# Performance work log

Measured on AMD Instinct MI355X. Metric: run time of the kernel, lower is better.

## Reference

```python
import jax, jax.numpy as jnp
import numpy as np

N_NODES = 100000


def _sage_conv(x, src, dst, Wl, bl, Wr):
    # PyG SAGEConv (aggr='mean', root_weight=True):
    # out_i = Wl @ mean_{j in N(i)} x_j + bl + Wr @ x_i
    msg = x[src]                                              # [E, F] gather
    s = jax.ops.segment_sum(msg, dst, num_segments=N_NODES)   # [N, F] scatter-add
    cnt = jax.ops.segment_sum(jnp.ones((src.shape[0], 1), x.dtype), dst,
                              num_segments=N_NODES)           # [N, 1]
    mean = s / jnp.maximum(cnt, 1.0)                          # empty nbhd -> 0
    return mean @ Wl + bl + x @ Wr


def setup_inputs() -> dict:
    key = jax.random.key(0)
    ks = jax.random.split(key, 8)
    N, E, F = N_NODES, 1600000, 128
    x = jax.random.normal(ks[0], (N, F), dtype=jnp.float32)
    edge_index = jax.random.randint(ks[1], (2, E), 0, N, dtype=jnp.int64)
    def lin(k, fi, fo):
        return jax.random.normal(k, (fi, fo), dtype=jnp.float32) / np.sqrt(fi)
    return {
        "x": x, "edge_index": edge_index,
        "Wl0": lin(ks[2], F, F), "bl0": jnp.zeros((F,), jnp.float32), "Wr0": lin(ks[3], F, F),
        "Wl1": lin(ks[4], F, F), "bl1": jnp.zeros((F,), jnp.float32), "Wr1": lin(ks[5], F, F),
        "Wl2": lin(ks[6], F, F), "bl2": jnp.zeros((F,), jnp.float32), "Wr2": lin(ks[7], F, F),
    }


def reference(x, edge_index, Wl0, bl0, Wr0, Wl1, bl1, Wr1, Wl2, bl2, Wr2):
    src, dst = edge_index[0], edge_index[1]
    # layers 0..num_layers-2: SAGEConv -> ReLU -> dropout(eval=identity)
    h = jax.nn.relu(_sage_conv(x, src, dst, Wl0, bl0, Wr0))
    h = jax.nn.relu(_sage_conv(h, src, dst, Wl1, bl1, Wr1))
    # final layer: no activation
    out = _sage_conv(h, src, dst, Wl2, bl2, Wr2)
    return out
```

## Files before the change

### kernel.cpp

```cpp
#include <hip/hip_runtime.h>
#include <stdint.h>

#define NN 100000
#define FF 128
#define NB 391

typedef __bf16 bf16x8 __attribute__((ext_vector_type(8)));
typedef float f32x4 __attribute__((ext_vector_type(4)));

__device__ __forceinline__ unsigned short f2bf(float f) {
    unsigned int u = __float_as_uint(f);
    u += 0x7FFF + ((u >> 16) & 1);
    return (unsigned short)(u >> 16);
}
__device__ __forceinline__ float bf2f(unsigned short b) {
    return __uint_as_float(((unsigned int)b) << 16);
}

__device__ __forceinline__ int edge_at(const void* ei, int idx, int is64) {
    if (is64) return (int)((const long long*)ei)[idx];
    return ((const int*)ei)[idx];
}

__global__ void init_kernel(const unsigned int* ei, int* flag, int* bcnt) {
    __shared__ int any;
    int t = threadIdx.x;
    if (t == 0) any = 0;
    for (int i = t; i < NB; i += 512) bcnt[i] = 0;
    __syncthreads();
    unsigned int v = ei[2 * t + 1];
    if (v != 0u) atomicOr(&any, 1);
    __syncthreads();
    if (t == 0) *flag = (any ? 0 : 1);
}

__global__ void bcount_prep_kernel(const void* ei, const int* flag, int* bcnt, int E,
                                   const float* __restrict__ x, unsigned short* __restrict__ xb,
                                   const float* Wl0, const float* Wr0,
                                   const float* Wl1, const float* Wr1,
                                   const float* Wl2, const float* Wr2,
                                   unsigned short* __restrict__ whi) {
    if (blockIdx.x < 256) {
        __shared__ int h[NB];
        for (int i = threadIdx.x; i < NB; i += 256) h[i] = 0;
        __syncthreads();
        int is64 = *flag;
        int stride = 256 * 256;
        for (int e = blockIdx.x * 256 + threadIdx.x; e < E; e += stride)
            atomicAdd(&h[edge_at(ei, E + e, is64) >> 8], 1);
        __syncthreads();
        for (int i = threadIdx.x; i < NB; i += 256) {
            int v = h[i];
            if (v) atomicAdd(&bcnt[i], v);
        }
    } else {
        int gid = (blockIdx.x - 256) * 256 + threadIdx.x;
        int gstride = (gridDim.x - 256) * 256;
        const int PC = NN * FF / 8;
        for (int i = gid; i < PC; i += gstride) {
            float4 a = ((const float4*)x)[i * 2];
            float4 b = ((const float4*)x)[i * 2 + 1];
            ushort4 p0 = make_ushort4(f2bf(a.x), f2bf(a.y), f2bf(a.z), f2bf(a.w));
            ushort4 p1 = make_ushort4(f2bf(b.x), f2bf(b.y), f2bf(b.z), f2bf(b.w));
            ((ushort4*)xb)[i * 2] = p0;
            ((ushort4*)xb)[i * 2 + 1] = p1;
        }
        const int WT = 3 * 256 * FF;
        for (int i = gid; i < WT; i += gstride) {
            int l = i >> 15;
            int rem = i & 32767;
            int n = rem >> 7;
            int k = rem & 127;
            const float* Wl = l == 0 ? Wl0 : (l == 1 ? Wl1 : Wl2);
            const float* Wr = l == 0 ? Wr0 : (l == 1 ? Wr1 : Wr2);
            float v = (n < FF) ? Wl[k * FF + n] : Wr[k * FF + (n - FF)];
            whi[i] = f2bf(v);
        }
    }
}

__global__ void bscan_kernel(const int* bcnt, int* bbase, int* bcursor,
                             int* rowptr, int E) {
    __shared__ int s[512];
    int t = threadIdx.x;
    int v = (t < NB) ? bcnt[t] : 0;
    s[t] = v;
    __syncthreads();
    for (int off = 1; off < 512; off <<= 1) {
        int u = (t >= off) ? s[t - off] : 0;
        __syncthreads();
        s[t] += u;
        __syncthreads();
    }
    if (t <= NB) {
        int excl = (t == 0) ? 0 : s[t - 1];
        bbase[t] = excl;
        if (t < NB) bcursor[t] = excl;
    }
    if (t == 0) rowptr[NN] = E;
}

__global__ void bscatter_kernel(const void* ei, const int* flag, int* bcursor,
                                unsigned int* packed, int E, int CH) {
    __shared__ int cnt[NB];
    __shared__ int base[NB];
    int t = threadIdx.x;
    for (int i = t; i < NB; i += 256) cnt[i] = 0;
    __syncthreads();
    int is64 = *flag;
    int beg = blockIdx.x * CH;
    int end = min(E, beg + CH);
    for (int e = beg + t; e < end; e += 256)
        atomicAdd(&cnt[edge_at(ei, E + e, is64) >> 8], 1);
    __syncthreads();
    for (int i = t; i < NB; i += 256) {
        int c = cnt[i];
        base[i] = c ? atomicAdd(&bcursor[i], c) : 0;
    }
    __syncthreads();
    for (int i = t; i < NB; i += 256) cnt[i] = 0;
    __syncthreads();
    for (int e = beg + t; e < end; e += 256) {
        int sV = edge_at(ei, e, is64);
        int d  = edge_at(ei, E + e, is64);
        int b = d >> 8;
        int pos = base[b] + atomicAdd(&cnt[b], 1);
        packed[pos] = ((unsigned int)sV << 8) | (unsigned int)(d & 255);
    }
}

__global__ void bfill_kernel(const unsigned int* __restrict__ packed,
                             const int* __restrict__ bbase,
                             int* __restrict__ rowptr, int* __restrict__ col) {
    __shared__ int cnt[256];
    __shared__ int scn[256];
    __shared__ int exc[256];
    int t = threadIdx.x;
    int b = blockIdx.x;
    int ebeg = bbase[b], eend = bbase[b + 1];
    cnt[t] = 0;
    __syncthreads();
    for (int e = ebeg + t; e < eend; e += 256)
        atomicAdd(&cnt[packed[e] & 255], 1);
    __syncthreads();
    int v = cnt[t];
    scn[t] = v;
    __syncthreads();
    for (int off = 1; off < 256; off <<= 1) {
        int u = (t >= off) ? scn[t - off] : 0;
        __syncthreads();
        scn[t] += u;
        __syncthreads();
    }
    int excl = scn[t] - v;
    exc[t] = excl;
    int node = b * 256 + t;
    if (node < NN) rowptr[node] = ebeg + excl;
    cnt[t] = 0;
    __syncthreads();
    for (int e = ebeg + t; e < eend; e += 256) {
        unsigned int p = packed[e];
        int l = p & 255;
        int pos = ebeg + exc[l] + atomicAdd(&cnt[l], 1);
        col[pos] = (int)(p >> 8);
    }
}

__device__ __forceinline__ unsigned int rowld(const unsigned short* __restrict__ h,
                                              int c, int lbyte) {
    return *(const unsigned int*)((const char*)h + ((size_t)(unsigned)c << 8) + lbyte);
}

__global__ void aggregate_kernel(const unsigned short* __restrict__ h,
                                 const int* __restrict__ rowptr,
                                 const int* __restrict__ col,
                                 unsigned short* __restrict__ m) {
    int gw = (int)((blockIdx.x * blockDim.x + threadIdx.x) >> 6);
    gw = __builtin_amdgcn_readfirstlane(gw);
    if (gw >= NN) return;
    const int lane = (int)(threadIdx.x & 63);
    const int lbyte = lane * 4;
    int beg = __builtin_amdgcn_readfirstlane(rowptr[gw]);
    int end = __builtin_amdgcn_readfirstlane(rowptr[gw + 1]);
    int deg = end - beg;
    float a0 = 0.f, a1 = 0.f;

    int done = 0;
    while (done < deg) {
        int batch = min(deg - done, 64);
        int colv = 0;
        if (lane < batch) colv = col[beg + done + lane];
        unsigned int u0 = 0, u1 = 0, u2 = 0, u3 = 0;
        u0 = rowld(h, __builtin_amdgcn_readlane(colv, 0), lbyte);
        if (batch > 1) u1 = rowld(h, __builtin_amdgcn_readlane(colv, 1), lbyte);
        if (batch > 2) u2 = rowld(h, __builtin_amdgcn_readlane(colv, 2), lbyte);
        if (batch > 3) u3 = rowld(h, __builtin_amdgcn_readlane(colv, 3), lbyte);
        for (int i = 0; i < batch; i += 4) {
            unsigned int n0 = 0, n1 = 0, n2 = 0, n3 = 0;
            if (i + 4 < batch) n0 = rowld(h, __builtin_amdgcn_readlane(colv, i + 4), lbyte);
            if (i + 5 < batch) n1 = rowld(h, __builtin_amdgcn_readlane(colv, i + 5), lbyte);
            if (i + 6 < batch) n2 = rowld(h, __builtin_amdgcn_readlane(colv, i + 6), lbyte);
            if (i + 7 < batch) n3 = rowld(h, __builtin_amdgcn_readlane(colv, i + 7), lbyte);
            a0 += __uint_as_float(u0 << 16);
            a1 += __uint_as_float(u0 & 0xffff0000u);
            a0 += __uint_as_float(u1 << 16);
            a1 += __uint_as_float(u1 & 0xffff0000u);
            a0 += __uint_as_float(u2 << 16);
            a1 += __uint_as_float(u2 & 0xffff0000u);
            a0 += __uint_as_float(u3 << 16);
            a1 += __uint_as_float(u3 & 0xffff0000u);
            u0 = n0; u1 = n1; u2 = n2; u3 = n3;
        }
        done += batch;
    }

    float r = deg > 0 ? 1.f / (float)deg : 0.f;
    unsigned int p = (unsigned int)f2bf(a0 * r) | ((unsigned int)f2bf(a1 * r) << 16);
    *(unsigned int*)((char*)m + ((size_t)gw << 8) + lbyte) = p;
}

template <int WMODE>
__global__ __launch_bounds__(256, 6) void gemm_mfma_kernel(
        const unsigned short* __restrict__ mb,
        const unsigned short* __restrict__ hb,
        const unsigned short* __restrict__ w2,
        const float* __restrict__ bl,
        void* __restrict__ outp) {
    __shared__ __align__(16) char smem[16384];

    const int t = threadIdx.x;
    const int lane = t & 63;
    const int wid = t >> 6;
    const int m0 = blockIdx.x * 64;
    const int n0w = wid * 32;

    f32x4 acc[4][2];
    #pragma unroll
    for (int mr = 0; mr < 4; ++mr)
        #pragma unroll
        for (int nr = 0; nr < 2; ++nr) acc[mr][nr] = (f32x4){0.f, 0.f, 0.f, 0.f};

    const int srow = t >> 2;
    const int sk8 = (t & 3) * 8;
    const int arow = lane & 15;
    const int kg = (lane >> 4) * 8;

    uint4 pfM, pfH;
    auto issueA = [&](int kc) {
        int gr = m0 + srow; if (gr >= NN) gr = NN - 1;
        size_t ga = (size_t)gr * FF + kc * 32 + sk8;
        pfM = *(const uint4*)(mb + ga);
        pfH = *(const uint4*)(hb + ga);
    };

    issueA(0);
    for (int kc = 0; kc < 4; ++kc) {
        __syncthreads();
        *(uint4*)(smem +        srow * 80 + sk8 * 2) = pfM;
        *(uint4*)(smem + 5120 + srow * 80 + sk8 * 2) = pfH;
        if (kc < 3) issueA(kc + 1);
        __syncthreads();

        bf16x8 wfrag[4];
        #pragma unroll
        for (int nr = 0; nr < 2; ++nr) {
            int n = n0w + nr * 16 + arow;
            wfrag[nr * 2 + 0] = *(const bf16x8*)(w2 + (size_t)n * FF + kc * 32 + kg);
            wfrag[nr * 2 + 1] = *(const bf16x8*)(w2 + (size_t)(128 + n) * FF + kc * 32 + kg);
        }
        const int kg2 = (lane >> 4) * 16;
        #pragma unroll
        for (int mr = 0; mr < 4; ++mr) {
            int row = mr * 16 + arow;
            bf16x8 a_m = *(const bf16x8*)(smem +        row * 80 + kg2);
            bf16x8 a_h = *(const bf16x8*)(smem + 5120 + row * 80 + kg2);
            #pragma unroll
            for (int nr = 0; nr < 2; ++nr) {
                acc[mr][nr] = __builtin_amdgcn_mfma_f32_16x16x32_bf16(wfrag[nr * 2 + 0], a_m, acc[mr][nr], 0, 0, 0);
                acc[mr][nr] = __builtin_amdgcn_mfma_f32_16x16x32_bf16(wfrag[nr * 2 + 1], a_h, acc[mr][nr], 0, 0, 0);
            }
        }
    }

    const int nodeL = lane & 15;
    const int rg4 = (lane >> 4) * 4;
    if (WMODE == 0) {
        __syncthreads();
        #pragma unroll
        for (int nr = 0; nr < 2; ++nr) {
            int n = n0w + nr * 16 + rg4;
            float4 bias = *(const float4*)(bl + n);
            int g = n >> 2;
            #pragma unroll
            for (int mr = 0; mr < 4; ++mr) {
                int row = mr * 16 + nodeL;
                f32x4 a = acc[mr][nr];
                float o0 = fmaxf(a[0] + bias.x, 0.f), o1 = fmaxf(a[1] + bias.y, 0.f);
                float o2 = fmaxf(a[2] + bias.z, 0.f), o3 = fmaxf(a[3] + bias.w, 0.f);
                ushort4 p = make_ushort4(f2bf(o0), f2bf(o1), f2bf(o2), f2bf(o3));
                *(ushort4*)(smem + row * 256 + ((g ^ ((row & 7) << 2)) << 3)) = p;
            }
        }
        __syncthreads();
        unsigned short* hout = (unsigned short*)outp;
        #pragma unroll
        for (int it = 0; it < 8; ++it) {
            int idx = t + it * 256;
            int row = idx >> 5;
            int g = idx & 31;
            int node = m0 + row;
            if (node < NN) {
                ushort4 v = *(const ushort4*)(smem + row * 256 + ((g ^ ((row & 7) << 2)) << 3));
                *(ushort4*)(hout + (size_t)node * FF + g * 4) = v;
            }
        }
    } else {
        float* fout = (float*)outp;
        #pragma unroll
        for (int r = 0; r < 2; ++r) {
            __syncthreads();
            #pragma unroll
            for (int nr = 0; nr < 2; ++nr) {
                int n = n0w + nr * 16 + rg4;
                float4 bias = *(const float4*)(bl + n);
                int g = n >> 2;
                #pragma unroll
                for (int mr = 2 * r; mr < 2 * r + 2; ++mr) {
                    int lrow = mr * 16 + nodeL - 32 * r;
                    f32x4 a = acc[mr][nr];
                    float4 p = make_float4(a[0] + bias.x, a[1] + bias.y,
                                           a[2] + bias.z, a[3] + bias.w);
                    *(float4*)(smem + lrow * 512 + ((g ^ (lrow & 7)) << 4)) = p;
                }
            }
            __syncthreads();
            #pragma unroll
            for (int it = 0; it < 4; ++it) {
                int idx = t + it * 256;
                int lrow = idx >> 5;
                int g = idx & 31;
                int node = m0 + 32 * r + lrow;
                if (node < NN) {
                    float4 v = *(const float4*)(smem + lrow * 512 + ((g ^ (lrow & 7)) << 4));
                    *(float4*)(fout + (size_t)node * FF + g * 4) = v;
                }
            }
        }
    }
}

extern "C" void kernel_launch(void* const* d_in, const int* in_sizes, int n_in,
                              void* d_out, int out_size, void* d_ws, size_t ws_size,
                              hipStream_t stream) {
    const float* x   = (const float*)d_in[0];
    const void*  ei  = d_in[1];
    const float* Wl0 = (const float*)d_in[2];
    const float* bl0 = (const float*)d_in[3];
    const float* Wr0 = (const float*)d_in[4];
    const float* Wl1 = (const float*)d_in[5];
    const float* bl1 = (const float*)d_in[6];
    const float* Wr1 = (const float*)d_in[7];
    const float* Wl2 = (const float*)d_in[8];
    const float* bl2 = (const float*)d_in[9];
    const float* Wr2 = (const float*)d_in[10];
    float* out = (float*)d_out;
    const int E = in_sizes[1] / 2;

    char* w = (char*)d_ws;
    size_t off = 0;
    auto alloc = [&](size_t bytes) {
        void* p = w + off;
        off += (bytes + 511) & ~(size_t)511;
        return p;
    };
    int*            flag    = (int*)alloc(4);
    int*            bcnt    = (int*)alloc(sizeof(int) * NB);
    int*            bbase   = (int*)alloc(sizeof(int) * (NB + 1));
    int*            bcursor = (int*)alloc(sizeof(int) * NB);
    int*            rowptr  = (int*)alloc(sizeof(int) * (NN + 1));
    unsigned int*   packed  = (unsigned int*)alloc(sizeof(int) * E);
    int*            col     = (int*)alloc(sizeof(int) * E);
    unsigned short* whi     = (unsigned short*)alloc(sizeof(short) * 3 * 256 * FF);
    unsigned short* xb      = (unsigned short*)alloc(sizeof(short) * (size_t)NN * FF);
    unsigned short* mbuf    = (unsigned short*)alloc(sizeof(short) * (size_t)NN * FF);
    unsigned short* hA      = (unsigned short*)alloc(sizeof(short) * (size_t)NN * FF);
    unsigned short* hB      = xb;

    init_kernel<<<1, 512, 0, stream>>>((const unsigned int*)ei, flag, bcnt);
    bcount_prep_kernel<<<1280, 256, 0, stream>>>(ei, flag, bcnt, E,
                                                 x, xb, Wl0, Wr0, Wl1, Wr1, Wl2, Wr2, whi);
    bscan_kernel<<<1, 512, 0, stream>>>(bcnt, bbase, bcursor, rowptr, E);
    int CH = (E + 255) / 256;
    bscatter_kernel<<<256, 256, 0, stream>>>(ei, flag, bcursor, packed, E, CH);
    bfill_kernel<<<NB, 256, 0, stream>>>(packed, bbase, rowptr, col);

    int gb = (NN + 63) / 64;
    int ab = (NN * 64 + 255) / 256;

    aggregate_kernel<<<ab, 256, 0, stream>>>(xb, rowptr, col, mbuf);
    gemm_mfma_kernel<0><<<gb, 256, 0, stream>>>(mbuf, xb, whi + 0 * 256 * FF, bl0, hA);
    aggregate_kernel<<<ab, 256, 0, stream>>>(hA, rowptr, col, mbuf);
    gemm_mfma_kernel<0><<<gb, 256, 0, stream>>>(mbuf, hA, whi + 1 * 256 * FF, bl1, hB);
    aggregate_kernel<<<ab, 256, 0, stream>>>(hB, rowptr, col, mbuf);
    gemm_mfma_kernel<1><<<gb, 256, 0, stream>>>(mbuf, hB, whi + 2 * 256 * FF, bl2, out);
}
```

Before: 309.0 us.

## Slice bf16 feature storage into 8 column slabs and aggregate per slab

Feature matrices are now stored as 8 slabs of 16 columns each (32 bytes per node), and the aggregate kernel assigns each block a single slab, so each slab's working set (about 3.2 MB) can stay resident in cache during the random gathers. Each wave now handles 8 destination nodes with 8 lanes each, and prefetches column indices with nontemporal loads up to the group's maximum degree. The GEMM's input loads and bf16 output writes are changed to the slab layout. In exchange, each gather is only 32 bytes wide, column indices are re-read once per slab, and lanes idle while their node waits on the highest-degree node in its group.

```diff
diff --git a/kernel.cpp b/kernel.cpp
--- a/kernel.cpp
+++ b/kernel.cpp
@@ -4,6 +4,8 @@
 #define NN 100000
 #define FF 128
 #define NB 391
+#define NSL 8
+#define SLW 16
 
 typedef __bf16 bf16x8 __attribute__((ext_vector_type(8)));
 typedef float f32x4 __attribute__((ext_vector_type(4)));
@@ -22,11 +24,13 @@
     return ((const int*)ei)[idx];
 }
 
-__global__ void init_kernel(const unsigned int* ei, int* flag, int* bcnt) {
+__global__ void init_kernel(const unsigned int* ei, int* flag, int* bcnt,
+                            int* col, int E) {
     __shared__ int any;
     int t = threadIdx.x;
     if (t == 0) any = 0;
     for (int i = t; i < NB; i += 512) bcnt[i] = 0;
+    if (t < 64) col[E + t] = 0;
     __syncthreads();
     unsigned int v = ei[2 * t + 1];
     if (v != 0u) atomicOr(&any, 1);
@@ -58,12 +62,16 @@
         int gstride = (gridDim.x - 256) * 256;
         const int PC = NN * FF / 8;
         for (int i = gid; i < PC; i += gstride) {
+            int n = i >> 4;
+            int ch = i & 15;
             float4 a = ((const float4*)x)[i * 2];
             float4 b = ((const float4*)x)[i * 2 + 1];
             ushort4 p0 = make_ushort4(f2bf(a.x), f2bf(a.y), f2bf(a.z), f2bf(a.w));
             ushort4 p1 = make_ushort4(f2bf(b.x), f2bf(b.y), f2bf(b.z), f2bf(b.w));
-            ((ushort4*)xb)[i * 2] = p0;
-            ((ushort4*)xb)[i * 2 + 1] = p1;
+            unsigned short* dst = xb + (size_t)(ch >> 1) * (NN * SLW)
+                                     + (size_t)n * SLW + (ch & 1) * 8;
+            ((ushort4*)dst)[0] = p0;
+            ((ushort4*)dst)[1] = p1;
         }
         const int WT = 3 * 256 * FF;
         for (int i = gid; i < WT; i += gstride) {
@@ -166,57 +174,64 @@
     }
 }
 
-__device__ __forceinline__ unsigned int rowld(const unsigned short* __restrict__ h,
-                                              int c, int lbyte) {
-    return *(const unsigned int*)((const char*)h + ((size_t)(unsigned)c << 8) + lbyte);
-}
-
 __global__ void aggregate_kernel(const unsigned short* __restrict__ h,
                                  const int* __restrict__ rowptr,
                                  const int* __restrict__ col,
                                  unsigned short* __restrict__ m) {
-    int gw = (int)((blockIdx.x * blockDim.x + threadIdx.x) >> 6);
-    gw = __builtin_amdgcn_readfirstlane(gw);
-    if (gw >= NN) return;
-    const int lane = (int)(threadIdx.x & 63);
-    const int lbyte = lane * 4;
-    int beg = __builtin_amdgcn_readfirstlane(rowptr[gw]);
-    int end = __builtin_amdgcn_readfirstlane(rowptr[gw + 1]);
-    int deg = end - beg;
+    const int s = blockIdx.x & 7;
+    const int tile = blockIdx.x >> 3;
+    const int t = threadIdx.x;
+    const int lane = t & 63;
+    const int g = lane >> 3;
+    const int L = lane & 7;
+    const int d = tile * 32 + (t >> 6) * 8 + g;
+
+    const char* hs = (const char*)h + (size_t)s * (NN * 32);
+    char*       msd = (char*)m + (size_t)s * (NN * 32);
+
+    int beg = rowptr[d];
+    int deg = rowptr[d + 1] - beg;
+    int degm1 = max(deg - 1, 0);
+
+    int dmax = deg;
+    dmax = max(dmax, __shfl_xor(dmax, 8));
+    dmax = max(dmax, __shfl_xor(dmax, 16));
+    dmax = max(dmax, __shfl_xor(dmax, 32));
+
+    auto CLD = [&](int i) -> int {
+        return __builtin_nontemporal_load(&col[beg + min(i, degm1)]);
+    };
+    auto GLD = [&](int c, int i) -> unsigned {
+        unsigned off = ((unsigned)c << 5) + (unsigned)(L << 2);
+        unsigned v = *(const unsigned*)(hs + off);
+        return (i < deg) ? v : 0u;
+    };
+
     float a0 = 0.f, a1 = 0.f;
 
-    int done = 0;
-    while (done < deg) {
-        int batch = min(deg - done, 64);
-        int colv = 0;
-        if (lane < batch) colv = col[beg + done + lane];
-        unsigned int u0 = 0, u1 = 0, u2 = 0, u3 = 0;
-        u0 = rowld(h, __builtin_amdgcn_readlane(colv, 0), lbyte);
-        if (batch > 1) u1 = rowld(h, __builtin_amdgcn_readlane(colv, 1), lbyte);
-        if (batch > 2) u2 = rowld(h, __builtin_amdgcn_readlane(colv, 2), lbyte);
-        if (batch > 3) u3 = rowld(h, __builtin_amdgcn_readlane(colv, 3), lbyte);
-        for (int i = 0; i < batch; i += 4) {
-            unsigned int n0 = 0, n1 = 0, n2 = 0, n3 = 0;
-            if (i + 4 < batch) n0 = rowld(h, __builtin_amdgcn_readlane(colv, i + 4), lbyte);
-            if (i + 5 < batch) n1 = rowld(h, __builtin_amdgcn_readlane(colv, i + 5), lbyte);
-            if (i + 6 < batch) n2 = rowld(h, __builtin_amdgcn_readlane(colv, i + 6), lbyte);
-            if (i + 7 < batch) n3 = rowld(h, __builtin_amdgcn_readlane(colv, i + 7), lbyte);
-            a0 += __uint_as_float(u0 << 16);
-            a1 += __uint_as_float(u0 & 0xffff0000u);
-            a0 += __uint_as_float(u1 << 16);
-            a1 += __uint_as_float(u1 & 0xffff0000u);
-            a0 += __uint_as_float(u2 << 16);
-            a1 += __uint_as_float(u2 & 0xffff0000u);
-            a0 += __uint_as_float(u3 << 16);
-            a1 += __uint_as_float(u3 & 0xffff0000u);
-            u0 = n0; u1 = n1; u2 = n2; u3 = n3;
-        }
-        done += batch;
+    int c0 = CLD(0), c1 = CLD(1), c2 = CLD(2), c3 = CLD(3);
+    int c4 = CLD(4), c5 = CLD(5), c6 = CLD(6), c7 = CLD(7);
+    unsigned u0 = GLD(c0, 0), u1 = GLD(c1, 1), u2 = GLD(c2, 2), u3 = GLD(c3, 3);
+    for (int i = 0; i < dmax; i += 4) {
+        int n0 = CLD(i + 8), n1 = CLD(i + 9), n2 = CLD(i + 10), n3 = CLD(i + 11);
+        unsigned w0 = GLD(c4, i + 4), w1 = GLD(c5, i + 5);
+        unsigned w2 = GLD(c6, i + 6), w3 = GLD(c7, i + 7);
+        a0 += __uint_as_float(u0 << 16);
+        a1 += __uint_as_float(u0 & 0xffff0000u);
+        a0 += __uint_as_float(u1 << 16);
+        a1 += __uint_as_float(u1 & 0xffff0000u);
+        a0 += __uint_as_float(u2 << 16);
+        a1 += __uint_as_float(u2 & 0xffff0000u);
+        a0 += __uint_as_float(u3 << 16);
+        a1 += __uint_as_float(u3 & 0xffff0000u);
+        u0 = w0; u1 = w1; u2 = w2; u3 = w3;
+        c4 = n0; c5 = n1; c6 = n2; c7 = n3;
     }
 
     float r = deg > 0 ? 1.f / (float)deg : 0.f;
-    unsigned int p = (unsigned int)f2bf(a0 * r) | ((unsigned int)f2bf(a1 * r) << 16);
-    *(unsigned int*)((char*)m + ((size_t)gw << 8) + lbyte) = p;
+    unsigned pk = (unsigned)f2bf(a0 * r) | ((unsigned)f2bf(a1 * r) << 16);
+    __builtin_nontemporal_store(pk,
+        (unsigned*)(msd + ((unsigned)d << 5) + (unsigned)(L << 2)));
 }
 
 template <int WMODE>
@@ -248,9 +263,10 @@
     uint4 pfM, pfH;
     auto issueA = [&](int kc) {
         int gr = m0 + srow; if (gr >= NN) gr = NN - 1;
-        size_t ga = (size_t)gr * FF + kc * 32 + sk8;
-        pfM = *(const uint4*)(mb + ga);
-        pfH = *(const uint4*)(hb + ga);
+        size_t soff = (size_t)(2 * kc + (sk8 >> 4)) * (NN * SLW)
+                    + (size_t)gr * SLW + (sk8 & 8);
+        pfM = *(const uint4*)(mb + soff);
+        pfH = *(const uint4*)(hb + soff);
     };
 
     issueA(0);
@@ -303,15 +319,15 @@
         }
         __syncthreads();
         unsigned short* hout = (unsigned short*)outp;
+        const int node_l = t >> 2;
+        const int sub = t & 3;
         #pragma unroll
         for (int it = 0; it < 8; ++it) {
-            int idx = t + it * 256;
-            int row = idx >> 5;
-            int g = idx & 31;
-            int node = m0 + row;
+            int g = it * 4 + sub;
+            int node = m0 + node_l;
             if (node < NN) {
-                ushort4 v = *(const ushort4*)(smem + row * 256 + ((g ^ ((row & 7) << 2)) << 3));
-                *(ushort4*)(hout + (size_t)node * FF + g * 4) = v;
+                ushort4 v = *(const ushort4*)(smem + node_l * 256 + ((g ^ ((node_l & 7) << 2)) << 3));
+                *(ushort4*)(hout + (size_t)it * (NN * SLW) + (size_t)node * SLW + sub * 4) = v;
             }
         }
     } else {
@@ -379,14 +395,14 @@
     int*            bcursor = (int*)alloc(sizeof(int) * NB);
     int*            rowptr  = (int*)alloc(sizeof(int) * (NN + 1));
     unsigned int*   packed  = (unsigned int*)alloc(sizeof(int) * E);
-    int*            col     = (int*)alloc(sizeof(int) * E);
+    int*            col     = (int*)alloc(sizeof(int) * (E + 64));
     unsigned short* whi     = (unsigned short*)alloc(sizeof(short) * 3 * 256 * FF);
     unsigned short* xb      = (unsigned short*)alloc(sizeof(short) * (size_t)NN * FF);
     unsigned short* mbuf    = (unsigned short*)alloc(sizeof(short) * (size_t)NN * FF);
     unsigned short* hA      = (unsigned short*)alloc(sizeof(short) * (size_t)NN * FF);
     unsigned short* hB      = xb;
 
-    init_kernel<<<1, 512, 0, stream>>>((const unsigned int*)ei, flag, bcnt);
+    init_kernel<<<1, 512, 0, stream>>>((const unsigned int*)ei, flag, bcnt, col, E);
     bcount_prep_kernel<<<1280, 256, 0, stream>>>(ei, flag, bcnt, E,
                                                  x, xb, Wl0, Wr0, Wl1, Wr1, Wl2, Wr2, whi);
     bscan_kernel<<<1, 512, 0, stream>>>(bcnt, bbase, bcursor, rowptr, E);
@@ -395,12 +411,12 @@
     bfill_kernel<<<NB, 256, 0, stream>>>(packed, bbase, rowptr, col);
 
     int gb = (NN + 63) / 64;
-    int ab = (NN * 64 + 255) / 256;
-
-    aggregate_kernel<<<ab, 256, 0, stream>>>(xb, rowptr, col, mbuf);
+    int ag = (NN / 32) * NSL;
+
+    aggregate_kernel<<<ag, 256, 0, stream>>>(xb, rowptr, col, mbuf);
     gemm_mfma_kernel<0><<<gb, 256, 0, stream>>>(mbuf, xb, whi + 0 * 256 * FF, bl0, hA);
-    aggregate_kernel<<<ab, 256, 0, stream>>>(hA, rowptr, col, mbuf);
+    aggregate_kernel<<<ag, 256, 0, stream>>>(hA, rowptr, col, mbuf);
     gemm_mfma_kernel<0><<<gb, 256, 0, stream>>>(mbuf, hA, whi + 1 * 256 * FF, bl1, hB);
-    aggregate_kernel<<<ab, 256, 0, stream>>>(hB, rowptr, col, mbuf);
+    aggregate_kernel<<<ag, 256, 0, stream>>>(hB, rowptr, col, mbuf);
     gemm_mfma_kernel<1><<<gb, 256, 0, stream>>>(mbuf, hB, whi + 2 * 256 * FF, bl2, out);
 }
```

New measurement: 682.5 us. 121% more time.
